# Kernel tuning notes

Measured on AMD Instinct MI355X. Metric: run time of the kernel, lower is better.

Reference implementation:

```python
import jax, jax.numpy as jnp
import numpy as np

B, H, S, D = 4, 16, 2048, 64
TEMPERATURE = 8.0  # sqrt(D)
MASK_FILL = -1e9


def setup_inputs() -> dict:
    key = jax.random.key(0)
    kq, kk, kv, km = jax.random.split(key, 4)
    q = jax.random.normal(kq, (B, H, S, D), dtype=jnp.float32)
    k = jax.random.normal(kk, (B, H, S, D), dtype=jnp.float32)
    v = jax.random.normal(kv, (B, H, S, D), dtype=jnp.float32)
    mask = jax.random.randint(km, (B, 1, 1, S), 0, 2, dtype=jnp.int32)
    return {"q": q, "k": k, "v": v, "mask": mask}


def reference(q, k, v, mask):
    # attn = (q / temperature) @ k^T  -> [B,H,S,S]
    attn = jnp.einsum('bhqd,bhkd->bhqk', q / TEMPERATURE, k)
    # mask-fill where mask == 0 (broadcasts over heads/query dim)
    attn = jnp.where(mask == 0, MASK_FILL, attn)
    # dropout is identity at inference (training=None in the original)
    # NOTE: the original module applies NO softmax; faithful reproduction.
    output = jnp.einsum('bhqk,bhkd->bhqd', attn, v)
    return (output, attn)
```

## Files before the change

### kernel.cpp

```cpp
#include <hip/hip_runtime.h>

constexpr int Bn = 4, Hn = 16, Sn = 2048, Dn = 64;
constexpr float MASK_FILL = -1e9f;

typedef __bf16 bf16x8 __attribute__((ext_vector_type(8)));
typedef __bf16 bf16x4 __attribute__((ext_vector_type(4)));
typedef float  f32x4  __attribute__((ext_vector_type(4)));
typedef int    i32x4  __attribute__((ext_vector_type(4)));

#define KSTRIDE 72
#define VSTRIDE 136

#define BARRIER_LGKM() asm volatile("s_waitcnt lgkmcnt(0)\n\ts_barrier" ::: "memory")

__global__ __launch_bounds__(256, 2) void attn_fused(
    const float* __restrict__ qg, const float* __restrict__ kg,
    const float* __restrict__ vg, const int* __restrict__ maskg,
    float* __restrict__ outg, float* __restrict__ attng)
{
  __shared__ __align__(16) __bf16 lds_k [128 * KSTRIDE];
  __shared__ __align__(16) __bf16 lds_vt[ 64 * VSTRIDE];
  __shared__ __align__(16) __bf16 lds_qs[128 * KSTRIDE];
  __shared__ __align__(16) int    lds_m [Sn];

  const int fid  = blockIdx.y * gridDim.x + blockIdx.x;
  const int nf   = ((fid & 7) << 7) | (fid >> 3);
  const int qt   = nf & 15;
  const int bh   = nf >> 4;
  const int b    = bh >> 4;
  const int tid  = threadIdx.x;
  const int wave = tid >> 6;
  const int lane = tid & 63;
  const int quad = lane >> 4;
  const int l16  = lane & 15;

  const int kt0  = nf & 15;

  const size_t hbase = (size_t)bh * Sn * Dn;
  const float* qp = qg + hbase + (size_t)qt * 128 * Dn;
  float* attnp = attng + (size_t)bh * Sn * Sn + (size_t)qt * 128 * (size_t)Sn;

  const int r0 = tid >> 4;
  const int c  = (tid & 15) << 2;

  {
    const int* mp = maskg + b * Sn;
    *(i32x4*)&lds_m[tid * 8]     = *(const i32x4*)(mp + tid * 8);
    *(i32x4*)&lds_m[tid * 8 + 4] = *(const i32x4*)(mp + tid * 8 + 4);
  }

#pragma unroll
  for (int i = 0; i < 8; ++i) {
    const int r = r0 + (i << 4);
    f32x4 val = __builtin_nontemporal_load((const f32x4*)(qp + r * Dn + c));
    bf16x4 pk;
    pk.x = (__bf16)(val.x * 0.125f);
    pk.y = (__bf16)(val.y * 0.125f);
    pk.z = (__bf16)(val.z * 0.125f);
    pk.w = (__bf16)(val.w * 0.125f);
    *(bf16x4*)&lds_qs[r * KSTRIDE + c] = pk;
  }

  f32x4 kpre[8], vpre[8];
  const float* kbase = kg + hbase;
  const float* vbase = vg + hbase;
  {
    const float* kp = kbase + (size_t)(kt0 * 128) * Dn;
    const float* vp = vbase + (size_t)(kt0 * 128) * Dn;
#pragma unroll
    for (int i = 0; i < 8; ++i) {
      kpre[i] = *(const f32x4*)(kp + (r0 + (i << 4)) * Dn + c);
      vpre[i] = *(const f32x4*)(vp + (r0 * 8 + i) * Dn + c);
    }
  }

  BARRIER_LGKM();

  bf16x8 qa[2][2];
#pragma unroll
  for (int qs = 0; qs < 2; ++qs)
#pragma unroll
    for (int ks = 0; ks < 2; ++ks)
      qa[qs][ks] = *(const bf16x8*)&lds_qs[(wave * 32 + qs * 16 + l16) * KSTRIDE + ks * 32 + quad * 8];

  __bf16* sbuf = &lds_qs[wave * 32 * KSTRIDE];

  f32x4 oacc[2][4];
#pragma unroll
  for (int qs = 0; qs < 2; ++qs)
#pragma unroll
    for (int ds = 0; ds < 4; ++ds)
      oacc[qs][ds] = (f32x4){0.f, 0.f, 0.f, 0.f};

  for (int it = 0; it < 16; ++it) {
    const int kt = (it + kt0) & 15;
    BARRIER_LGKM();

#pragma unroll
    for (int i = 0; i < 8; ++i) {
      const int r = r0 + (i << 4);
      f32x4 kv = kpre[i];
      bf16x4 pk;
      pk.x = (__bf16)kv.x; pk.y = (__bf16)kv.y;
      pk.z = (__bf16)kv.z; pk.w = (__bf16)kv.w;
      *(bf16x4*)&lds_k[r * KSTRIDE + c] = pk;
    }
#pragma unroll
    for (int j = 0; j < 4; ++j) {
      bf16x8 t;
#pragma unroll
      for (int i = 0; i < 8; ++i)
        t[i] = (__bf16)vpre[i][j];
      *(bf16x8*)&lds_vt[(c + j) * VSTRIDE + r0 * 8] = t;
    }

    BARRIER_LGKM();

    if (it < 15) {
      const int ktn = (it + 1 + kt0) & 15;
      const float* kp = kbase + (size_t)(ktn * 128) * Dn;
      const float* vp = vbase + (size_t)(ktn * 128) * Dn;
#pragma unroll
      for (int i = 0; i < 8; ++i) {
        kpre[i] = *(const f32x4*)(kp + (r0 + (i << 4)) * Dn + c);
        vpre[i] = *(const f32x4*)(vp + (r0 * 8 + i) * Dn + c);
      }
    }

    f32x4 sacc[2][8];
#pragma unroll
    for (int ns = 0; ns < 8; ++ns) {
      bf16x8 ka0 = *(const bf16x8*)&lds_k[(ns * 16 + l16) * KSTRIDE +      quad * 8];
      bf16x8 ka1 = *(const bf16x8*)&lds_k[(ns * 16 + l16) * KSTRIDE + 32 + quad * 8];
      const i32x4 m4 = *(const i32x4*)&lds_m[kt * 128 + ns * 16 + quad * 4];
#pragma unroll
      for (int qs = 0; qs < 2; ++qs) {
        f32x4 acc = (f32x4){0.f, 0.f, 0.f, 0.f};
        acc = __builtin_amdgcn_mfma_f32_16x16x32_bf16(ka0, qa[qs][0], acc, 0, 0, 0);
        acc = __builtin_amdgcn_mfma_f32_16x16x32_bf16(ka1, qa[qs][1], acc, 0, 0, 0);
        acc.x = m4.x ? acc.x : MASK_FILL;
        acc.y = m4.y ? acc.y : MASK_FILL;
        acc.z = m4.z ? acc.z : MASK_FILL;
        acc.w = m4.w ? acc.w : MASK_FILL;
        sacc[qs][ns] = acc;
        const int row = wave * 32 + qs * 16 + l16;
        *(f32x4*)(attnp + (size_t)row * Sn + kt * 128 + ns * 16 + quad * 4) = acc;
      }
    }

#pragma unroll
    for (int half = 0; half < 2; ++half) {
#pragma unroll
      for (int ns4 = 0; ns4 < 4; ++ns4) {
        const int ns = half * 4 + ns4;
#pragma unroll
        for (int qs = 0; qs < 2; ++qs) {
          f32x4 sv = sacc[qs][ns];
          bf16x4 sb;
          sb.x = (__bf16)sv.x; sb.y = (__bf16)sv.y;
          sb.z = (__bf16)sv.z; sb.w = (__bf16)sv.w;
          *(bf16x4*)&sbuf[(qs * 16 + l16) * KSTRIDE + ns4 * 16 + quad * 4] = sb;
        }
      }
      asm volatile("" ::: "memory");
#pragma unroll
      for (int ks = 0; ks < 2; ++ks) {
        bf16x8 sb0 = *(const bf16x8*)&sbuf[(     l16) * KSTRIDE + ks * 32 + quad * 8];
        bf16x8 sb1 = *(const bf16x8*)&sbuf[(16 + l16) * KSTRIDE + ks * 32 + quad * 8];
#pragma unroll
        for (int ds = 0; ds < 4; ++ds) {
          bf16x8 va = *(const bf16x8*)&lds_vt[(ds * 16 + l16) * VSTRIDE + half * 64 + ks * 32 + quad * 8];
          oacc[0][ds] = __builtin_amdgcn_mfma_f32_16x16x32_bf16(va, sb0, oacc[0][ds], 0, 0, 0);
          oacc[1][ds] = __builtin_amdgcn_mfma_f32_16x16x32_bf16(va, sb1, oacc[1][ds], 0, 0, 0);
        }
      }
      asm volatile("" ::: "memory");
    }
  }

  float* op = outg + hbase + (size_t)qt * 128 * Dn;
#pragma unroll
  for (int qs = 0; qs < 2; ++qs)
#pragma unroll
    for (int ds = 0; ds < 4; ++ds) {
      const int row = wave * 32 + qs * 16 + l16;
      __builtin_nontemporal_store(oacc[qs][ds],
          (f32x4*)(op + (size_t)row * Dn + ds * 16 + quad * 4));
    }
}

extern "C" void kernel_launch(void* const* d_in, const int* in_sizes, int n_in,
                              void* d_out, int out_size, void* d_ws, size_t ws_size,
                              hipStream_t stream) {
  const float* q    = (const float*)d_in[0];
  const float* k    = (const float*)d_in[1];
  const float* v    = (const float*)d_in[2];
  const int*   mask = (const int*)d_in[3];
  float* out  = (float*)d_out;
  float* attn = out + (size_t)Bn * Hn * Sn * Dn;

  dim3 grid(Sn / 128, Bn * Hn);
  attn_fused<<<grid, 256, 0, stream>>>(q, k, v, mask, out, attn);
}
```

Baseline: 1.218 ms.

## Pre-convert K and V to bf16 in a workspace kernel before fused attention

```diff
diff --git a/kernel.cpp b/kernel.cpp
--- a/kernel.cpp
+++ b/kernel.cpp
@@ -2,6 +2,7 @@
 
 constexpr int Bn = 4, Hn = 16, Sn = 2048, Dn = 64;
 constexpr float MASK_FILL = -1e9f;
+constexpr size_t KV_ELEMS = (size_t)Bn * Hn * Sn * Dn;
 
 typedef __bf16 bf16x8 __attribute__((ext_vector_type(8)));
 typedef __bf16 bf16x4 __attribute__((ext_vector_type(4)));
@@ -13,10 +14,32 @@
 
 #define BARRIER_LGKM() asm volatile("s_waitcnt lgkmcnt(0)\n\ts_barrier" ::: "memory")
 
+__global__ __launch_bounds__(256) void convert_kv(
+    const float* __restrict__ kg, const float* __restrict__ vg,
+    __bf16* __restrict__ kb, __bf16* __restrict__ vb)
+{
+  const size_t n4 = KV_ELEMS / 4;
+  const size_t stride = (size_t)gridDim.x * 256;
+  for (size_t i = (size_t)blockIdx.x * 256 + threadIdx.x; i < n4; i += stride) {
+    f32x4 kv = __builtin_nontemporal_load((const f32x4*)(kg + i * 4));
+    bf16x4 pk;
+    pk.x = (__bf16)kv.x; pk.y = (__bf16)kv.y;
+    pk.z = (__bf16)kv.z; pk.w = (__bf16)kv.w;
+    *(bf16x4*)(kb + i * 4) = pk;
+    f32x4 vv = __builtin_nontemporal_load((const f32x4*)(vg + i * 4));
+    bf16x4 pv;
+    pv.x = (__bf16)vv.x; pv.y = (__bf16)vv.y;
+    pv.z = (__bf16)vv.z; pv.w = (__bf16)vv.w;
+    *(bf16x4*)(vb + i * 4) = pv;
+  }
+}
+
+template <bool PRE>
 __global__ __launch_bounds__(256, 2) void attn_fused(
     const float* __restrict__ qg, const float* __restrict__ kg,
     const float* __restrict__ vg, const int* __restrict__ maskg,
-    float* __restrict__ outg, float* __restrict__ attng)
+    float* __restrict__ outg, float* __restrict__ attng,
+    const __bf16* __restrict__ kbg, const __bf16* __restrict__ vbg)
 {
   __shared__ __align__(16) __bf16 lds_k [128 * KSTRIDE];
   __shared__ __align__(16) __bf16 lds_vt[ 64 * VSTRIDE];
@@ -61,16 +84,23 @@
     *(bf16x4*)&lds_qs[r * KSTRIDE + c] = pk;
   }
 
-  f32x4 kpre[8], vpre[8];
-  const float* kbase = kg + hbase;
-  const float* vbase = vg + hbase;
+  f32x4  kpre [8], vpre [8];
+  bf16x4 kpreb[8], vpreb[8];
+  const float*  kbase  = kg  + hbase;
+  const float*  vbase  = vg  + hbase;
+  const __bf16* kbbase = PRE ? (kbg + hbase) : nullptr;
+  const __bf16* vbbase = PRE ? (vbg + hbase) : nullptr;
   {
-    const float* kp = kbase + (size_t)(kt0 * 128) * Dn;
-    const float* vp = vbase + (size_t)(kt0 * 128) * Dn;
+    const size_t toff = (size_t)(kt0 * 128) * Dn;
 #pragma unroll
     for (int i = 0; i < 8; ++i) {
-      kpre[i] = *(const f32x4*)(kp + (r0 + (i << 4)) * Dn + c);
-      vpre[i] = *(const f32x4*)(vp + (r0 * 8 + i) * Dn + c);
+      if constexpr (PRE) {
+        kpreb[i] = *(const bf16x4*)(kbbase + toff + (r0 + (i << 4)) * Dn + c);
+        vpreb[i] = *(const bf16x4*)(vbbase + toff + (r0 * 8 + i) * Dn + c);
+      } else {
+        kpre[i] = *(const f32x4*)(kbase + toff + (r0 + (i << 4)) * Dn + c);
+        vpre[i] = *(const f32x4*)(vbase + toff + (r0 * 8 + i) * Dn + c);
+      }
     }
   }
 
@@ -99,18 +129,22 @@
 #pragma unroll
     for (int i = 0; i < 8; ++i) {
       const int r = r0 + (i << 4);
-      f32x4 kv = kpre[i];
-      bf16x4 pk;
-      pk.x = (__bf16)kv.x; pk.y = (__bf16)kv.y;
-      pk.z = (__bf16)kv.z; pk.w = (__bf16)kv.w;
-      *(bf16x4*)&lds_k[r * KSTRIDE + c] = pk;
+      if constexpr (PRE) {
+        *(bf16x4*)&lds_k[r * KSTRIDE + c] = kpreb[i];
+      } else {
+        f32x4 kv = kpre[i];
+        bf16x4 pk;
+        pk.x = (__bf16)kv.x; pk.y = (__bf16)kv.y;
+        pk.z = (__bf16)kv.z; pk.w = (__bf16)kv.w;
+        *(bf16x4*)&lds_k[r * KSTRIDE + c] = pk;
+      }
     }
 #pragma unroll
     for (int j = 0; j < 4; ++j) {
       bf16x8 t;
 #pragma unroll
       for (int i = 0; i < 8; ++i)
-        t[i] = (__bf16)vpre[i][j];
+        t[i] = PRE ? vpreb[i][j] : (__bf16)vpre[i][j];
       *(bf16x8*)&lds_vt[(c + j) * VSTRIDE + r0 * 8] = t;
     }
 
@@ -118,12 +152,16 @@
 
     if (it < 15) {
       const int ktn = (it + 1 + kt0) & 15;
-      const float* kp = kbase + (size_t)(ktn * 128) * Dn;
-      const float* vp = vbase + (size_t)(ktn * 128) * Dn;
+      const size_t toff = (size_t)(ktn * 128) * Dn;
 #pragma unroll
       for (int i = 0; i < 8; ++i) {
-        kpre[i] = *(const f32x4*)(kp + (r0 + (i << 4)) * Dn + c);
-        vpre[i] = *(const f32x4*)(vp + (r0 * 8 + i) * Dn + c);
+        if constexpr (PRE) {
+          kpreb[i] = *(const bf16x4*)(kbbase + toff + (r0 + (i << 4)) * Dn + c);
+          vpreb[i] = *(const bf16x4*)(vbbase + toff + (r0 * 8 + i) * Dn + c);
+        } else {
+          kpre[i] = *(const f32x4*)(kbase + toff + (r0 + (i << 4)) * Dn + c);
+          vpre[i] = *(const f32x4*)(vbase + toff + (r0 * 8 + i) * Dn + c);
+        }
       }
     }
 
@@ -144,7 +182,8 @@
         acc.w = m4.w ? acc.w : MASK_FILL;
         sacc[qs][ns] = acc;
         const int row = wave * 32 + qs * 16 + l16;
-        *(f32x4*)(attnp + (size_t)row * Sn + kt * 128 + ns * 16 + quad * 4) = acc;
+        __builtin_nontemporal_store(acc,
+            (f32x4*)(attnp + (size_t)row * Sn + kt * 128 + ns * 16 + quad * 4));
       }
     }
 
@@ -200,5 +239,13 @@
   float* attn = out + (size_t)Bn * Hn * Sn * Dn;
 
   dim3 grid(Sn / 128, Bn * Hn);
-  attn_fused<<<grid, 256, 0, stream>>>(q, k, v, mask, out, attn);
+  const size_t need = KV_ELEMS * 2 * sizeof(__bf16);
+  if (d_ws != nullptr && ws_size >= need) {
+    __bf16* kb = (__bf16*)d_ws;
+    __bf16* vb = kb + KV_ELEMS;
+    convert_kv<<<2048, 256, 0, stream>>>(k, v, kb, vb);
+    attn_fused<true><<<grid, 256, 0, stream>>>(q, k, v, mask, out, attn, kb, vb);
+  } else {
+    attn_fused<false><<<grid, 256, 0, stream>>>(q, k, v, mask, out, attn, nullptr, nullptr);
+  }
 }
```

After: 1.327 ms. 1.09x slower.
